# Performance work log

Hardware: AMD Instinct MI355X
Metric: run time of the kernel (lower is better)

## Reference

```python
import jax, jax.numpy as jnp
import numpy as np

B, S, D, H, R = 4, 1024, 1024, 16, 4
HD = D // H
EPS = 1e-5


def layer_norm(x, g, b):
    mu = jnp.mean(x, axis=-1, keepdims=True)
    var = jnp.mean(jnp.square(x - mu), axis=-1, keepdims=True)
    return (x - mu) * jax.lax.rsqrt(var + EPS) * g + b


def setup_inputs() -> dict:
    key = jax.random.key(0)
    ks = jax.random.split(key, 12)
    sd = 1.0 / np.sqrt(D)
    sf = 1.0 / np.sqrt(R * D)
    inp = {
        "x": jax.random.normal(ks[0], (B, S, D), jnp.float32),
        "ln1_g": jnp.ones((D,), jnp.float32),
        "ln1_b": jnp.zeros((D,), jnp.float32),
        "wq": jax.random.uniform(ks[1], (D, D), jnp.float32, -sd, sd),
        "bq": jnp.zeros((D,), jnp.float32),
        "wk": jax.random.uniform(ks[2], (D, D), jnp.float32, -sd, sd),
        "bk": jnp.zeros((D,), jnp.float32),
        "wv": jax.random.uniform(ks[3], (D, D), jnp.float32, -sd, sd),
        "bv": jnp.zeros((D,), jnp.float32),
        "wo": jax.random.uniform(ks[4], (D, D), jnp.float32, -sd, sd),
        "bo": jnp.zeros((D,), jnp.float32),
        "ln2_g": jnp.ones((D,), jnp.float32),
        "ln2_b": jnp.zeros((D,), jnp.float32),
        "w1": jax.random.uniform(ks[5], (D, R * D), jnp.float32, -sd, sd),
        "b1": jnp.zeros((R * D,), jnp.float32),
        "w2": jax.random.uniform(ks[6], (R * D, D), jnp.float32, -sf, sf),
        "b2": jnp.zeros((D,), jnp.float32),
    }
    return inp


def reference(x, ln1_g, ln1_b, wq, bq, wk, bk, wv, bv, wo, bo,
              ln2_g, ln2_b, w1, b1, w2, b2):
    # Pre-LN MHA. Per-head Q/K/V linears concatenated == one batched projection
    # reshaped into heads, so we batch all heads in single GEMMs.
    h = layer_norm(x, ln1_g, ln1_b)
    q = (h @ wq + bq).reshape(B, S, H, HD)
    k = (h @ wk + bk).reshape(B, S, H, HD)
    v = (h @ wv + bv).reshape(B, S, H, HD)
    scores = jnp.einsum("bqhd,bkhd->bhqk", q, k) / np.sqrt(HD)
    attn = jax.nn.softmax(scores, axis=-1)
    ctx = jnp.einsum("bhqk,bkhd->bqhd", attn, v).reshape(B, S, D)
    x = x + ctx @ wo + bo
    # Pre-LN MLP with exact (erf) GELU, matching torch nn.GELU default.
    h2 = layer_norm(x, ln2_g, ln2_b)
    mlp = jax.nn.gelu(h2 @ w1 + b1, approximate=False) @ w2 + b2
    return x + mlp
```

## Files before the change

### kernel.cpp

```cpp
#include <hip/hip_runtime.h>

typedef unsigned short u16;
typedef __attribute__((ext_vector_type(8))) __bf16 bf16x8;
typedef __attribute__((ext_vector_type(4))) float floatx4;

#define FLAG_F32OUT  1
#define FLAG_GELU    2
#define FLAG_PARTIAL 4

__device__ __forceinline__ u16 f2bf(float f) {
  union { float f; unsigned u; } un;
  un.f = f;
  unsigned u = un.u;
  u += 0x7fffu + ((u >> 16) & 1u);
  return (u16)(u >> 16);
}

__device__ __forceinline__ float gelu_f(float x) {
  float t = 1.5957691216f * (x + 0.044715f * x * x * x);
  return x / (1.0f + __expf(-t));
}

__device__ __forceinline__ floatx4 mfma16(bf16x8 a, bf16x8 b, floatx4 c) {
  return __builtin_amdgcn_mfma_f32_16x16x32_bf16(a, b, c, 0, 0, 0);
}

__device__ __forceinline__ void glds16(const void* g, void* l) {
  __builtin_amdgcn_global_load_lds(
      (__attribute__((address_space(1))) unsigned int*)(void*)g,
      (__attribute__((address_space(3))) unsigned int*)l, 16, 0, 0);
}

__global__ __launch_bounds__(256) void transpose_bf16(
    const float* __restrict__ W, u16* __restrict__ Wt, int K, int N,
    float scale) {
  __shared__ float tile[32][33];
  int n0 = blockIdx.x * 32, k0 = blockIdx.y * 32;
  int tx = threadIdx.x, ty = threadIdx.y;
#pragma unroll
  for (int i = 0; i < 4; ++i)
    tile[ty + i * 8][tx] = W[(size_t)(k0 + ty + i * 8) * N + n0 + tx];
  __syncthreads();
#pragma unroll
  for (int i = 0; i < 4; ++i)
    Wt[(size_t)(n0 + ty + i * 8) * K + k0 + tx] =
        f2bf(tile[tx][ty + i * 8] * scale);
}

__global__ __launch_bounds__(256) void concat_bias(
    const float* __restrict__ bq, const float* __restrict__ bk,
    const float* __restrict__ bv, float* __restrict__ o) {
  int i = blockIdx.x * 256 + threadIdx.x;
  float v = (i < 1024) ? bq[i] * 0.125f : (i < 2048 ? bk[i - 1024] : bv[i - 2048]);
  o[i] = v;
}

__global__ __launch_bounds__(256) void ln_kernel(
    const float* __restrict__ x, const float* __restrict__ g,
    const float* __restrict__ b, u16* __restrict__ out) {
  int row = blockIdx.x;
  int tid = threadIdx.x;
  const float4* xr = (const float4*)(x + (size_t)row * 1024);
  float4 v = xr[tid];
  float s = v.x + v.y + v.z + v.w;
  float s2 = v.x * v.x + v.y * v.y + v.z * v.z + v.w * v.w;
#pragma unroll
  for (int m = 32; m >= 1; m >>= 1) {
    s += __shfl_xor(s, m, 64);
    s2 += __shfl_xor(s2, m, 64);
  }
  __shared__ float red[8];
  int wave = tid >> 6, lane = tid & 63;
  if (lane == 0) { red[wave] = s; red[4 + wave] = s2; }
  __syncthreads();
  s = red[0] + red[1] + red[2] + red[3];
  s2 = red[4] + red[5] + red[6] + red[7];
  float mu = s * (1.0f / 1024.0f);
  float var = s2 * (1.0f / 1024.0f) - mu * mu;
  float inv = rsqrtf(var + 1e-5f);
  float4 gv = ((const float4*)g)[tid];
  float4 bv = ((const float4*)b)[tid];
  ushort4 ov;
  ov.x = f2bf((v.x - mu) * inv * gv.x + bv.x);
  ov.y = f2bf((v.y - mu) * inv * gv.y + bv.y);
  ov.z = f2bf((v.z - mu) * inv * gv.z + bv.z);
  ov.w = f2bf((v.w - mu) * inv * gv.w + bv.w);
  *(ushort4*)(out + (size_t)row * 1024 + tid * 4) = ov;
}

__global__ __launch_bounds__(256, 4) void gemm_bt(
    const u16* __restrict__ A, const u16* __restrict__ Bt,
    const float* __restrict__ bias,
    void* __restrict__ outp, void* __restrict__ outp2,
    int M, int N, int K, int Ks, int flags) {
  __shared__ __align__(16) u16 smem[17408];
  u16* As = smem;
  u16* Bs = smem + 8192;
  int tid = threadIdx.x;
  int lane = tid & 63, wave = tid >> 6;
  int lm = lane & 15, quad = lane >> 4;
  int wm = (wave >> 1) * 64, wn = (wave & 1) * 64;
  int bm = blockIdx.x, bn = blockIdx.y;
  int koff = blockIdx.z * Ks;

  const u16* aP = A + (size_t)(bm * 128 + (tid >> 2)) * K + koff + (tid & 3) * 8;
  const u16* bP = Bt + (size_t)(bn * 128 + (tid >> 2)) * K + koff + (tid & 3) * 8;
  u16* asD = As + tid * 8;
  u16* bsD = Bs + tid * 8;
  size_t rstep = (size_t)64 * K;

  floatx4 acc[4][4];
#pragma unroll
  for (int i = 0; i < 4; ++i)
#pragma unroll
    for (int j = 0; j < 4; ++j) acc[i][j] = (floatx4){0.f, 0.f, 0.f, 0.f};

  for (int k0 = 0; k0 < Ks; k0 += 64) {
#pragma unroll
    for (int p = 0; p < 2; ++p) {
      glds16(aP + p * 32, asD + p * 4096);
      glds16(aP + p * 32 + rstep, asD + p * 4096 + 2048);
      glds16(bP + p * 32, bsD + p * 4096);
      glds16(bP + p * 32 + rstep, bsD + p * 4096 + 2048);
    }
    aP += 64;
    bP += 64;
    __syncthreads();
#pragma unroll
    for (int p = 0; p < 2; ++p) {
      bf16x8 af[4], bfr[4];
#pragma unroll
      for (int mi = 0; mi < 4; ++mi)
        af[mi] = *(const bf16x8*)&As[p * 4096 + (wm + mi * 16 + lm) * 32 + quad * 8];
#pragma unroll
      for (int ni = 0; ni < 4; ++ni)
        bfr[ni] = *(const bf16x8*)&Bs[p * 4096 + (wn + ni * 16 + lm) * 32 + quad * 8];
#pragma unroll
      for (int mi = 0; mi < 4; ++mi)
#pragma unroll
        for (int ni = 0; ni < 4; ++ni)
          acc[mi][ni] = mfma16(af[mi], bfr[ni], acc[mi][ni]);
    }
    __syncthreads();
  }

  bool gelu = (flags & FLAG_GELU) != 0;
  bool part = (flags & FLAG_PARTIAL) != 0;
  bool f32p = part || ((flags & FLAG_F32OUT) != 0);
  void* op = blockIdx.z ? outp2 : outp;

  if (!f32p) {
    u16* Ct = smem;
#pragma unroll
    for (int ni = 0; ni < 4; ++ni) {
      int col = bn * 128 + wn + ni * 16 + lm;
      float bv = part ? 0.0f : bias[col];
#pragma unroll
      for (int mi = 0; mi < 4; ++mi) {
        int lr0 = wm + mi * 16 + quad * 4;
#pragma unroll
        for (int r = 0; r < 4; ++r) {
          float vv = acc[mi][ni][r] + bv;
          if (gelu) vv = gelu_f(vv);
          Ct[(lr0 + r) * 136 + wn + ni * 16 + lm] = f2bf(vv);
        }
      }
    }
    __syncthreads();
#pragma unroll
    for (int p = 0; p < 8; ++p) {
      int unit = p * 256 + tid;
      int row = unit >> 4, ch = unit & 15;
      uint4 v = *(const uint4*)&Ct[row * 136 + ch * 8];
      *(uint4*)&((u16*)op)[(size_t)(bm * 128 + row) * N + bn * 128 + ch * 8] = v;
    }
  } else {
    float* Cf = (float*)smem;
#pragma unroll
    for (int pp = 0; pp < 2; ++pp) {
      __syncthreads();
      if ((wave >> 1) == pp) {
#pragma unroll
        for (int ni = 0; ni < 4; ++ni) {
          int col = bn * 128 + wn + ni * 16 + lm;
          float bv = part ? 0.0f : bias[col];
#pragma unroll
          for (int mi = 0; mi < 4; ++mi) {
            int lr0 = mi * 16 + quad * 4;
#pragma unroll
            for (int r = 0; r < 4; ++r) {
              float vv = acc[mi][ni][r] + bv;
              if (gelu) vv = gelu_f(vv);
              Cf[(lr0 + r) * 132 + wn + ni * 16 + lm] = vv;
            }
          }
        }
      }
      __syncthreads();
#pragma unroll
      for (int p = 0; p < 8; ++p) {
        int unit = p * 256 + tid;
        int row = unit >> 5, ch = unit & 31;
        float4 v = *(const float4*)&Cf[row * 132 + ch * 4];
        size_t gi = (size_t)(bm * 128 + pp * 64 + row) * N + bn * 128 + ch * 4;
        *(float4*)&((float*)op)[gi] = v;
      }
    }
  }
}

__global__ __launch_bounds__(512) void flash_attn(
    const u16* __restrict__ qkv, u16* __restrict__ ctx) {
  __shared__ __align__(16) u16 Qs[128 * 72];
  __shared__ __align__(16) u16 Ks[64 * 72];
  __shared__ __align__(16) u16 Vt[64 * 64];

  int tid = threadIdx.x;
  int lane = tid & 63, wave = tid >> 6;
  int lm = lane & 15, quad = lane >> 4;
  int qt = blockIdx.x & 7;
  int hh = (blockIdx.x >> 3) & 15;
  int b = blockIdx.x >> 7;

  int krow = tid >> 3;
  int col8 = (tid & 7) * 8;
  int cb = col8 >> 3;

  size_t base_q = ((size_t)(b * 1024 + qt * 128)) * 3072 + hh * 64;
#pragma unroll
  for (int r = 0; r < 2; ++r) {
    int idx = r * 512 + tid;
    int row = idx >> 3;
    int c8 = (idx & 7) * 8;
    *(uint4*)&Qs[row * 72 + c8] =
        *(const uint4*)&qkv[base_q + (size_t)row * 3072 + c8];
  }
  __syncthreads();
  bf16x8 a0 = *(const bf16x8*)&Qs[(wave * 16 + lm) * 72 + quad * 8];
  bf16x8 a1 = *(const bf16x8*)&Qs[(wave * 16 + lm) * 72 + 32 + quad * 8];
  u16* Ps = &Qs[wave * 16 * 72];

  float l_r[4];
  floatx4 acc[4];
#pragma unroll
  for (int r = 0; r < 4; ++r) l_r[r] = 0.0f;
#pragma unroll
  for (int d = 0; d < 4; ++d) acc[d] = (floatx4){0.f, 0.f, 0.f, 0.f};

  size_t kv0 = ((size_t)(b * 1024 + krow)) * 3072 + 1024 + hh * 64 + col8;
  const size_t kv_step = (size_t)64 * 3072;

  uint4 kreg = *(const uint4*)&qkv[kv0];
  uint4 vreg = *(const uint4*)&qkv[kv0 + 1024];

  int rw = krow >> 3;
  int rl = krow & 7;

  for (int j = 0; j < 16; ++j) {
    __syncthreads();
    *(uint4*)&Ks[krow * 72 + col8] = kreg;
    {
      u16* ve = (u16*)&vreg;
#pragma unroll
      for (int e = 0; e < 8; ++e) {
        int d = col8 + e;
        int chunk = (rw ^ cb ^ e) & 7;
        Vt[d * 64 + chunk * 8 + rl] = ve[e];
      }
    }
    __syncthreads();

    if (j < 15) {
      size_t kvn = kv0 + (size_t)(j + 1) * kv_step;
      kreg = *(const uint4*)&qkv[kvn];
      vreg = *(const uint4*)&qkv[kvn + 1024];
    }

    floatx4 sacc[4];
#pragma unroll
    for (int ni = 0; ni < 4; ++ni) {
      bf16x8 b0 = *(const bf16x8*)&Ks[(ni * 16 + lm) * 72 + quad * 8];
      bf16x8 b1 = *(const bf16x8*)&Ks[(ni * 16 + lm) * 72 + 32 + quad * 8];
      floatx4 z = (floatx4){0.f, 0.f, 0.f, 0.f};
      z = mfma16(a0, b0, z);
      z = mfma16(a1, b1, z);
      sacc[ni] = z;
    }

#pragma unroll
    for (int r = 0; r < 4; ++r) {
      float p0 = __expf(sacc[0][r]);
      float p1 = __expf(sacc[1][r]);
      float p2 = __expf(sacc[2][r]);
      float p3 = __expf(sacc[3][r]);
      l_r[r] += (p0 + p1) + (p2 + p3);
      Ps[(quad * 4 + r) * 72 + 0 * 16 + lm] = f2bf(p0);
      Ps[(quad * 4 + r) * 72 + 1 * 16 + lm] = f2bf(p1);
      Ps[(quad * 4 + r) * 72 + 2 * 16 + lm] = f2bf(p2);
      Ps[(quad * 4 + r) * 72 + 3 * 16 + lm] = f2bf(p3);
    }

    bf16x8 pa0 = *(const bf16x8*)&Ps[lm * 72 + quad * 8];
    bf16x8 pa1 = *(const bf16x8*)&Ps[lm * 72 + 32 + quad * 8];
#pragma unroll
    for (int dd = 0; dd < 4; ++dd) {
      int d = dd * 16 + lm;
      int dx = ((d >> 3) ^ d) & 7;
      bf16x8 vb0 = *(const bf16x8*)&Vt[d * 64 + ((quad ^ dx) & 7) * 8];
      bf16x8 vb1 = *(const bf16x8*)&Vt[d * 64 + (((4 + quad) ^ dx) & 7) * 8];
      acc[dd] = mfma16(pa0, vb0, acc[dd]);
      acc[dd] = mfma16(pa1, vb1, acc[dd]);
    }
  }

  float rl4[4];
#pragma unroll
  for (int r = 0; r < 4; ++r) {
    float sm = l_r[r];
#pragma unroll
    for (int mm = 1; mm < 16; mm <<= 1) sm += __shfl_xor(sm, mm, 64);
    rl4[r] = 1.0f / sm;
  }
#pragma unroll
  for (int dd = 0; dd < 4; ++dd)
#pragma unroll
    for (int r = 0; r < 4; ++r)
      Ps[(quad * 4 + r) * 72 + dd * 16 + lm] = f2bf(acc[dd][r] * rl4[r]);
  size_t obase = (size_t)(b * 1024 + qt * 128 + wave * 16);
#pragma unroll
  for (int p = 0; p < 2; ++p) {
    int unit = p * 64 + lane;
    int row = unit >> 3, ch = unit & 7;
    uint4 v = *(const uint4*)&Ps[row * 72 + ch * 8];
    *(uint4*)&ctx[(obase + row) * 1024 + hh * 64 + ch * 8] = v;
  }
}

__global__ __launch_bounds__(256) void reduce_ln(
    float* __restrict__ x2, const float* __restrict__ p1,
    const float* __restrict__ x, const float* __restrict__ bo,
    const float* __restrict__ g, const float* __restrict__ bb,
    u16* __restrict__ h2) {
  int row = blockIdx.x, tid = threadIdx.x;
  size_t base = (size_t)row * 256;
  float4 a = ((const float4*)x2)[base + tid];
  float4 p = ((const float4*)p1)[base + tid];
  float4 c = ((const float4*)x)[base + tid];
  float4 d = ((const float4*)bo)[tid];
  float4 o;
  o.x = a.x + p.x + c.x + d.x;
  o.y = a.y + p.y + c.y + d.y;
  o.z = a.z + p.z + c.z + d.z;
  o.w = a.w + p.w + c.w + d.w;
  ((float4*)x2)[base + tid] = o;

  float s = o.x + o.y + o.z + o.w;
  float s2 = o.x * o.x + o.y * o.y + o.z * o.z + o.w * o.w;
#pragma unroll
  for (int m = 32; m >= 1; m >>= 1) {
    s += __shfl_xor(s, m, 64);
    s2 += __shfl_xor(s2, m, 64);
  }
  __shared__ float red[8];
  int wave = tid >> 6, lane = tid & 63;
  if (lane == 0) { red[wave] = s; red[4 + wave] = s2; }
  __syncthreads();
  s = red[0] + red[1] + red[2] + red[3];
  s2 = red[4] + red[5] + red[6] + red[7];
  float mu = s * (1.0f / 1024.0f);
  float var = s2 * (1.0f / 1024.0f) - mu * mu;
  float inv = rsqrtf(var + 1e-5f);
  float4 gv = ((const float4*)g)[tid];
  float4 bv = ((const float4*)bb)[tid];
  ushort4 ov;
  ov.x = f2bf((o.x - mu) * inv * gv.x + bv.x);
  ov.y = f2bf((o.y - mu) * inv * gv.y + bv.y);
  ov.z = f2bf((o.z - mu) * inv * gv.z + bv.z);
  ov.w = f2bf((o.w - mu) * inv * gv.w + bv.w);
  *(ushort4*)(h2 + (size_t)row * 1024 + tid * 4) = ov;
}

__global__ __launch_bounds__(256) void reduce4(
    float* __restrict__ out, const float* __restrict__ p1,
    const float* __restrict__ resid, const float* __restrict__ bias) {
  int i = blockIdx.x * 256 + threadIdx.x;
  float4 a = ((const float4*)out)[i];
  float4 b = ((const float4*)p1)[i];
  float4 c = ((const float4*)resid)[i];
  float4 d = ((const float4*)bias)[i & 255];
  float4 o;
  o.x = a.x + b.x + c.x + d.x;
  o.y = a.y + b.y + c.y + d.y;
  o.z = a.z + b.z + c.z + d.z;
  o.w = a.w + b.w + c.w + d.w;
  ((float4*)out)[i] = o;
}

extern "C" void kernel_launch(void* const* d_in, const int* in_sizes, int n_in,
                              void* d_out, int out_size, void* d_ws, size_t ws_size,
                              hipStream_t stream) {
  const float* x    = (const float*)d_in[0];
  const float* ln1g = (const float*)d_in[1];
  const float* ln1b = (const float*)d_in[2];
  const float* wq   = (const float*)d_in[3];
  const float* bq   = (const float*)d_in[4];
  const float* wk   = (const float*)d_in[5];
  const float* bk   = (const float*)d_in[6];
  const float* wv   = (const float*)d_in[7];
  const float* bv   = (const float*)d_in[8];
  const float* wo   = (const float*)d_in[9];
  const float* bo   = (const float*)d_in[10];
  const float* ln2g = (const float*)d_in[11];
  const float* ln2b = (const float*)d_in[12];
  const float* w1   = (const float*)d_in[13];
  const float* b1   = (const float*)d_in[14];
  const float* w2   = (const float*)d_in[15];
  const float* b2   = (const float*)d_in[16];

  char* ws = (char*)d_ws;
  const size_t MB = 1024ull * 1024ull;
  u16*   h     = (u16*)(ws + 0 * MB);
  u16*   h2    = (u16*)(ws + 0 * MB);
  u16*   qkv   = (u16*)(ws + 8 * MB);
  float* pwo   = (float*)(ws + 8 * MB);
  u16*   act   = (u16*)(ws + 8 * MB);
  u16*   ctxb  = (u16*)(ws + 32 * MB);
  float* bqkv  = (float*)(ws + 32 * MB);
  float* x2    = (float*)(ws + 40 * MB);
  float* pw2   = (float*)(ws + 56 * MB);
  u16*   wqkvt = (u16*)(ws + 64 * MB);
  u16*   wot   = (u16*)(ws + 70 * MB);
  u16*   w1t   = (u16*)(ws + 72 * MB);
  u16*   w2t   = (u16*)(ws + 80 * MB);

  dim3 tb(32, 8);
  transpose_bf16<<<dim3(32, 32), tb, 0, stream>>>(wq, wqkvt, 1024, 1024, 0.125f);
  transpose_bf16<<<dim3(32, 32), tb, 0, stream>>>(wk, wqkvt + 1024 * 1024, 1024, 1024, 1.0f);
  transpose_bf16<<<dim3(32, 32), tb, 0, stream>>>(wv, wqkvt + 2 * 1024 * 1024, 1024, 1024, 1.0f);
  transpose_bf16<<<dim3(32, 32), tb, 0, stream>>>(wo, wot, 1024, 1024, 1.0f);
  transpose_bf16<<<dim3(128, 32), tb, 0, stream>>>(w1, w1t, 1024, 4096, 1.0f);
  transpose_bf16<<<dim3(32, 128), tb, 0, stream>>>(w2, w2t, 4096, 1024, 1.0f);
  concat_bias<<<12, 256, 0, stream>>>(bq, bk, bv, bqkv);

  ln_kernel<<<4096, 256, 0, stream>>>(x, ln1g, ln1b, h);

  gemm_bt<<<dim3(32, 24, 1), 256, 0, stream>>>(
      h, wqkvt, bqkv, (void*)qkv, nullptr, 4096, 3072, 1024, 1024, 0);

  flash_attn<<<512, 512, 0, stream>>>(qkv, ctxb);

  gemm_bt<<<dim3(32, 8, 2), 256, 0, stream>>>(
      ctxb, wot, nullptr, (void*)x2, (void*)pwo, 4096, 1024, 1024, 512,
      FLAG_PARTIAL);
  reduce_ln<<<4096, 256, 0, stream>>>(x2, pwo, x, bo, ln2g, ln2b, h2);

  gemm_bt<<<dim3(32, 32, 1), 256, 0, stream>>>(
      h2, w1t, b1, (void*)act, nullptr, 4096, 4096, 1024, 1024, FLAG_GELU);

  gemm_bt<<<dim3(32, 8, 2), 256, 0, stream>>>(
      act, w2t, nullptr, d_out, (void*)pw2, 4096, 1024, 4096, 2048,
      FLAG_PARTIAL);
  reduce4<<<4096, 256, 0, stream>>>((float*)d_out, pw2, x2, b2);
}
```

Baseline: 347.4 us.

## Merge weight-prep kernels and use 4-way bf16 split-K for the W2 GEMM

Folds the six weight transpose launches and the bias concat into one prep kernel dispatched by block index, which cuts launch overhead. The final MLP down-projection goes from 2-way to 4-way split-K, so 1024 blocks run instead of 512 and the device is better occupied. Partials from slices 1-3 are stored as bf16 to halve the extra partial traffic, and the reduce kernel sums them in fp32. Rounding partial sums to bf16 adds some precision loss to the output.

```diff
diff --git a/kernel.cpp b/kernel.cpp
--- a/kernel.cpp
+++ b/kernel.cpp
@@ -7,6 +7,7 @@
 #define FLAG_F32OUT  1
 #define FLAG_GELU    2
 #define FLAG_PARTIAL 4
+#define FLAG_PBF16   8
 
 __device__ __forceinline__ u16 f2bf(float f) {
   union { float f; unsigned u; } un;
@@ -16,6 +17,12 @@
   return (u16)(u >> 16);
 }
 
+__device__ __forceinline__ float bf2f(u16 h) {
+  union { unsigned u; float f; } un;
+  un.u = ((unsigned)h) << 16;
+  return un.f;
+}
+
 __device__ __forceinline__ float gelu_f(float x) {
   float t = 1.5957691216f * (x + 0.044715f * x * x * x);
   return x / (1.0f + __expf(-t));
@@ -31,12 +38,44 @@
       (__attribute__((address_space(3))) unsigned int*)l, 16, 0, 0);
 }
 
-__global__ __launch_bounds__(256) void transpose_bf16(
-    const float* __restrict__ W, u16* __restrict__ Wt, int K, int N,
-    float scale) {
+__global__ __launch_bounds__(256) void prep_all(
+    const float* __restrict__ wq, const float* __restrict__ wk,
+    const float* __restrict__ wv, const float* __restrict__ wo,
+    const float* __restrict__ w1, const float* __restrict__ w2,
+    const float* __restrict__ bq, const float* __restrict__ bk,
+    const float* __restrict__ bv,
+    u16* __restrict__ wqkvt, u16* __restrict__ wot,
+    u16* __restrict__ w1t, u16* __restrict__ w2t,
+    float* __restrict__ bqkv) {
+  int b = blockIdx.x;
+  int tx = threadIdx.x, ty = threadIdx.y;
+  if (b >= 12288) {
+    int i = (b - 12288) * 256 + ty * 32 + tx;
+    float v = (i < 1024) ? bq[i] * 0.125f
+                         : (i < 2048 ? bk[i - 1024] : bv[i - 2048]);
+    bqkv[i] = v;
+    return;
+  }
+  const float* W;
+  u16* Wt;
+  int K, N, bx, by;
+  float scale = 1.0f;
+  if (b < 4096) {
+    int w = b >> 10, t = b & 1023;
+    bx = t & 31; by = t >> 5; K = 1024; N = 1024;
+    if (w == 0)      { W = wq; Wt = wqkvt;                scale = 0.125f; }
+    else if (w == 1) { W = wk; Wt = wqkvt + 1024 * 1024; }
+    else if (w == 2) { W = wv; Wt = wqkvt + 2 * 1024 * 1024; }
+    else             { W = wo; Wt = wot; }
+  } else if (b < 8192) {
+    int t = b - 4096;
+    bx = t & 127; by = t >> 7; K = 1024; N = 4096; W = w1; Wt = w1t;
+  } else {
+    int t = b - 8192;
+    bx = t & 31; by = t >> 5; K = 4096; N = 1024; W = w2; Wt = w2t;
+  }
   __shared__ float tile[32][33];
-  int n0 = blockIdx.x * 32, k0 = blockIdx.y * 32;
-  int tx = threadIdx.x, ty = threadIdx.y;
+  int n0 = bx * 32, k0 = by * 32;
 #pragma unroll
   for (int i = 0; i < 4; ++i)
     tile[ty + i * 8][tx] = W[(size_t)(k0 + ty + i * 8) * N + n0 + tx];
@@ -45,14 +84,6 @@
   for (int i = 0; i < 4; ++i)
     Wt[(size_t)(n0 + ty + i * 8) * K + k0 + tx] =
         f2bf(tile[tx][ty + i * 8] * scale);
-}
-
-__global__ __launch_bounds__(256) void concat_bias(
-    const float* __restrict__ bq, const float* __restrict__ bk,
-    const float* __restrict__ bv, float* __restrict__ o) {
-  int i = blockIdx.x * 256 + threadIdx.x;
-  float v = (i < 1024) ? bq[i] * 0.125f : (i < 2048 ? bk[i - 1024] : bv[i - 2048]);
-  o[i] = v;
 }
 
 __global__ __launch_bounds__(256) void ln_kernel(
@@ -146,8 +177,15 @@
 
   bool gelu = (flags & FLAG_GELU) != 0;
   bool part = (flags & FLAG_PARTIAL) != 0;
-  bool f32p = part || ((flags & FLAG_F32OUT) != 0);
-  void* op = blockIdx.z ? outp2 : outp;
+  bool pbf = (flags & FLAG_PBF16) != 0;
+  bool f32p = ((flags & FLAG_F32OUT) != 0) ||
+              (part && !(pbf && blockIdx.z > 0));
+  void* op;
+  if (blockIdx.z == 0)
+    op = outp;
+  else
+    op = (char*)outp2 +
+         (size_t)(blockIdx.z - 1) * M * N * (pbf ? 2 : 4);
 
   if (!f32p) {
     u16* Ct = smem;
@@ -380,19 +418,21 @@
   *(ushort4*)(h2 + (size_t)row * 1024 + tid * 4) = ov;
 }
 
-__global__ __launch_bounds__(256) void reduce4(
-    float* __restrict__ out, const float* __restrict__ p1,
+__global__ __launch_bounds__(256) void reduce4b(
+    float* __restrict__ out, const u16* __restrict__ pb,
     const float* __restrict__ resid, const float* __restrict__ bias) {
   int i = blockIdx.x * 256 + threadIdx.x;
   float4 a = ((const float4*)out)[i];
-  float4 b = ((const float4*)p1)[i];
+  ushort4 q0 = ((const ushort4*)pb)[i];
+  ushort4 q1 = ((const ushort4*)(pb + 4194304))[i];
+  ushort4 q2 = ((const ushort4*)(pb + 8388608))[i];
   float4 c = ((const float4*)resid)[i];
   float4 d = ((const float4*)bias)[i & 255];
   float4 o;
-  o.x = a.x + b.x + c.x + d.x;
-  o.y = a.y + b.y + c.y + d.y;
-  o.z = a.z + b.z + c.z + d.z;
-  o.w = a.w + b.w + c.w + d.w;
+  o.x = a.x + bf2f(q0.x) + bf2f(q1.x) + bf2f(q2.x) + c.x + d.x;
+  o.y = a.y + bf2f(q0.y) + bf2f(q1.y) + bf2f(q2.y) + c.y + d.y;
+  o.z = a.z + bf2f(q0.z) + bf2f(q1.z) + bf2f(q2.z) + c.z + d.z;
+  o.w = a.w + bf2f(q0.w) + bf2f(q1.w) + bf2f(q2.w) + c.w + d.w;
   ((float4*)out)[i] = o;
 }
 
@@ -427,20 +467,14 @@
   u16*   ctxb  = (u16*)(ws + 32 * MB);
   float* bqkv  = (float*)(ws + 32 * MB);
   float* x2    = (float*)(ws + 40 * MB);
-  float* pw2   = (float*)(ws + 56 * MB);
+  u16*   pw2   = (u16*)(ws + 56 * MB);
   u16*   wqkvt = (u16*)(ws + 64 * MB);
   u16*   wot   = (u16*)(ws + 70 * MB);
   u16*   w1t   = (u16*)(ws + 72 * MB);
   u16*   w2t   = (u16*)(ws + 80 * MB);
 
-  dim3 tb(32, 8);
-  transpose_bf16<<<dim3(32, 32), tb, 0, stream>>>(wq, wqkvt, 1024, 1024, 0.125f);
-  transpose_bf16<<<dim3(32, 32), tb, 0, stream>>>(wk, wqkvt + 1024 * 1024, 1024, 1024, 1.0f);
-  transpose_bf16<<<dim3(32, 32), tb, 0, stream>>>(wv, wqkvt + 2 * 1024 * 1024, 1024, 1024, 1.0f);
-  transpose_bf16<<<dim3(32, 32), tb, 0, stream>>>(wo, wot, 1024, 1024, 1.0f);
-  transpose_bf16<<<dim3(128, 32), tb, 0, stream>>>(w1, w1t, 1024, 4096, 1.0f);
-  transpose_bf16<<<dim3(32, 128), tb, 0, stream>>>(w2, w2t, 4096, 1024, 1.0f);
-  concat_bias<<<12, 256, 0, stream>>>(bq, bk, bv, bqkv);
+  prep_all<<<12300, dim3(32, 8), 0, stream>>>(
+      wq, wk, wv, wo, w1, w2, bq, bk, bv, wqkvt, wot, w1t, w2t, bqkv);
 
   ln_kernel<<<4096, 256, 0, stream>>>(x, ln1g, ln1b, h);
 
@@ -457,8 +491,8 @@
   gemm_bt<<<dim3(32, 32, 1), 256, 0, stream>>>(
       h2, w1t, b1, (void*)act, nullptr, 4096, 4096, 1024, 1024, FLAG_GELU);
 
-  gemm_bt<<<dim3(32, 8, 2), 256, 0, stream>>>(
-      act, w2t, nullptr, d_out, (void*)pw2, 4096, 1024, 4096, 2048,
-      FLAG_PARTIAL);
-  reduce4<<<4096, 256, 0, stream>>>((float*)d_out, pw2, x2, b2);
-}
+  gemm_bt<<<dim3(32, 8, 4), 256, 0, stream>>>(
+      act, w2t, nullptr, d_out, (void*)pw2, 4096, 1024, 4096, 1024,
+      FLAG_PARTIAL | FLAG_PBF16);
+  reduce4b<<<4096, 256, 0, stream>>>((float*)d_out, pw2, x2, b2);
+}
```

After: 326.5 us. -6.0%, faster.
